# Optimization experiments

Hardware: AMD Instinct MI355X
Metric: run time of the kernel (lower is better)

The kernel has to match this reference:

```python
import math
import jax, jax.numpy as jnp
import numpy as np

B, S, D, H, DK = 2, 2048, 1024, 16, 64
NUM_BUCKETS, MAX_DISTANCE = 32, 128


def _relative_position_bucket(rel_pos):
    # bidirectional=True (encoder): is_decoder=False
    nb = NUM_BUCKETS // 2
    rel_buckets = (rel_pos > 0).astype(jnp.int32) * nb
    rp = jnp.abs(rel_pos)
    max_exact = nb // 2
    is_small = rp < max_exact
    rp_large = max_exact + (
        jnp.log(rp.astype(jnp.float32) / max_exact)
        / math.log(MAX_DISTANCE / max_exact)
        * (nb - max_exact)
    ).astype(jnp.int32)
    rp_large = jnp.minimum(rp_large, nb - 1)
    return rel_buckets + jnp.where(is_small, rp, rp_large)


def compute_bias(rel_bias, q_len, k_len):
    ctx = jnp.arange(q_len, dtype=jnp.int32)[:, None]
    mem = jnp.arange(k_len, dtype=jnp.int32)[None, :]
    buckets = _relative_position_bucket(mem - ctx)          # [q,k]
    vals = rel_bias[buckets]                                 # [q,k,H]
    return jnp.transpose(vals, (2, 0, 1))[None]              # [1,H,q,k]


def setup_inputs() -> dict:
    key = jax.random.key(0)
    ks = jax.random.split(key, 6)
    scale = 0.02
    return {
        "hidden_states": jax.random.normal(ks[0], (B, S, D), jnp.float32),
        "Wq": jax.random.normal(ks[1], (D, H * DK), jnp.float32) * scale,
        "Wk": jax.random.normal(ks[2], (D, H * DK), jnp.float32) * scale,
        "Wv": jax.random.normal(ks[3], (D, H * DK), jnp.float32) * scale,
        "Wo": jax.random.normal(ks[4], (H * DK, D), jnp.float32) * scale,
        "rel_bias": jax.random.normal(ks[5], (NUM_BUCKETS, H), jnp.float32) * scale,
    }


def reference(hidden_states, Wq, Wk, Wv, Wo, rel_bias):
    b, s, _ = hidden_states.shape

    def shape(x):  # [b,s,H*DK] -> [b,H,s,DK]
        return x.reshape(b, s, H, DK).transpose(0, 2, 1, 3)

    q = shape(hidden_states @ Wq)
    k = shape(hidden_states @ Wk)
    v = shape(hidden_states @ Wv)

    # T5: no 1/sqrt(d_k) scaling
    scores = jnp.einsum("bhqd,bhkd->bhqk", q, k)
    position_bias = compute_bias(rel_bias, s, s)             # [1,H,s,s]
    scores = scores + position_bias
    attn = jax.nn.softmax(scores.astype(jnp.float32), axis=-1).astype(scores.dtype)
    out = jnp.einsum("bhqk,bhkd->bhqd", attn, v)
    out = out.transpose(0, 2, 1, 3).reshape(b, s, H * DK)
    return out @ Wo
```

## Files before the change

### kernel.cpp

```cpp
#include <hip/hip_runtime.h>

#define HH 16
#define DKK 64
#define SS 2048
#define BB 2
#define DD 1024

typedef __attribute__((ext_vector_type(4))) float f32x4;
typedef __attribute__((ext_vector_type(16))) float f32x16;
typedef __attribute__((ext_vector_type(8))) short bf16x8;
typedef __attribute__((ext_vector_type(4))) short s16x4;
typedef __attribute__((ext_vector_type(4))) int i32x4;

#define WAITCNT_VM0 0xF70

__device__ __forceinline__ short bf16b(float f) {
    union { float f; unsigned u; } x; x.f = f;
    unsigned r = (x.u + 0x7fffu + ((x.u >> 16) & 1u)) >> 16;
    return (short)r;
}

__device__ __forceinline__ f32x4 mfma16(bf16x8 a, bf16x8 b, f32x4 c) {
    return __builtin_amdgcn_mfma_f32_16x16x32_bf16(a, b, c, 0, 0, 0);
}

__device__ __forceinline__ f32x16 mfma32(bf16x8 a, bf16x8 b, f32x16 c) {
    return __builtin_amdgcn_mfma_f32_32x32x16_bf16(a, b, c, 0, 0, 0);
}

__device__ __forceinline__ void lds16(const short* g, short* l) {
    __builtin_amdgcn_global_load_lds(
        (const __attribute__((address_space(1))) void*)g,
        (__attribute__((address_space(3))) void*)l, 16, 0, 0);
}

__device__ __forceinline__ int cvtpk(float lo, float hi) {
    int r;
    asm("v_cvt_pk_bf16_f32 %0, %1, %2" : "=v"(r) : "v"(lo), "v"(hi));
    return r;
}

__device__ __forceinline__ void swap32(int& a, int& b) {
    asm("v_permlane32_swap_b32 %0, %1" : "+v"(a), "+v"(b));
}

__global__ __launch_bounds__(256) void prep(
    const float* __restrict__ hs,
    const float* __restrict__ W0, const float* __restrict__ W1,
    const float* __restrict__ W2, const float* __restrict__ W3,
    const float* __restrict__ rb,
    short* __restrict__ hsb,
    short* __restrict__ T0, short* __restrict__ T1,
    short* __restrict__ T2, short* __restrict__ T3,
    float* __restrict__ tab) {
    __shared__ short tile[32][33];
    int blk = blockIdx.x, tid = threadIdx.x;
    if (blk < 4096) {
        int i = (blk * 256 + tid) * 4;
        f32x4 v = *(const f32x4*)(hs + i);
        s16x4 o;
        o.x = bf16b(v.x); o.y = bf16b(v.y); o.z = bf16b(v.z); o.w = bf16b(v.w);
        *(s16x4*)(hsb + i) = o;
    } else if (blk < 8192) {
        int t = blk - 4096;
        int z = t >> 10, r = t & 1023;
        int bx = r & 31, by = r >> 5;
        const float* W; short* T;
        switch (z) {
            case 0: W = W0; T = T0; break;
            case 1: W = W1; T = T1; break;
            case 2: W = W2; T = T2; break;
            default: W = W3; T = T3; break;
        }
        int n0 = bx * 32, k0 = by * 32;
        int tx = tid & 31, ty = (tid >> 5) * 4;
#pragma unroll
        for (int i = 0; i < 4; i++)
            tile[ty + i][tx] = bf16b(W[(k0 + ty + i) * DD + n0 + tx]);
        __syncthreads();
#pragma unroll
        for (int i = 0; i < 4; i++)
            T[(n0 + ty + i) * DD + k0 + tx] = tile[tx][ty + i];
    } else {
        int idx = (blk - 8192) * 256 + tid;
        if (idx < HH * 4095) {
            int h = idx / 4095, d = idx % 4095;
            int rel = d - 2047;
            int bucket = (rel > 0) ? 16 : 0;
            unsigned rr = (rel < 0) ? (unsigned)(-rel) : (unsigned)rel;
            int add;
            if (rr < 8) add = (int)rr;
            else {
                int e = 31 - __clz(rr);
                unsigned long long r2 = (unsigned long long)rr * (unsigned long long)rr;
                int f = 2 * e + ((r2 >= (2ull << (2 * e))) ? 1 : 0);
                add = 8 + (f - 6);
                if (add > 15) add = 15;
            }
            bucket += add;
            tab[h * 4095 + d] = rb[bucket * HH + h] * 1.44269504f;
        }
    }
}

__global__ __launch_bounds__(256) void gemm_qkv(
    const short* __restrict__ A, const short* __restrict__ Wt,
    short* __restrict__ Cq, short* __restrict__ Ck, short* __restrict__ Cvt) {
    const int K = 1024;
    __shared__ short As[128 * 32];
    __shared__ short Bs[128 * 32];
    int tid = threadIdx.x;
    int wave = tid >> 6, lane = tid & 63;
    int quad = lane >> 4, l16 = lane & 15;
    int m0 = blockIdx.y * 128, n0 = blockIdx.x * 128;

    int wm = (wave & 1) * 64, wn = (wave >> 1) * 64;
    int r0 = tid >> 2, c0 = (tid & 3) * 8;

    f32x4 acc[4][4];
#pragma unroll
    for (int i = 0; i < 4; i++)
#pragma unroll
        for (int j = 0; j < 4; j++) acc[i][j] = (f32x4){0.f, 0.f, 0.f, 0.f};

    for (int k0 = 0; k0 < K; k0 += 32) {
        __syncthreads();
        lds16(A + (size_t)(m0 + r0) * K + k0 + c0, As + wave * 512);
        lds16(A + (size_t)(m0 + 64 + r0) * K + k0 + c0, As + 2048 + wave * 512);
        lds16(Wt + (size_t)(n0 + r0) * K + k0 + c0, Bs + wave * 512);
        lds16(Wt + (size_t)(n0 + 64 + r0) * K + k0 + c0, Bs + 2048 + wave * 512);
        __syncthreads();
        bf16x8 af[4], bfr[4];
#pragma unroll
        for (int t = 0; t < 4; t++) {
            af[t] = *(const bf16x8*)(As + (wm + t * 16 + l16) * 32 + quad * 8);
            bfr[t] = *(const bf16x8*)(Bs + (wn + t * 16 + l16) * 32 + quad * 8);
        }
#pragma unroll
        for (int mt = 0; mt < 4; mt++)
#pragma unroll
            for (int nt = 0; nt < 4; nt++)
                acc[mt][nt] = mfma16(af[mt], bfr[nt], acc[mt][nt]);
    }

#pragma unroll
    for (int mt = 0; mt < 4; mt++) {
#pragma unroll
        for (int nt = 0; nt < 4; nt++) {
#pragma unroll
            for (int r = 0; r < 4; r++) {
                int gm = m0 + wm + mt * 16 + quad * 4 + r;
                int gn = n0 + wn + nt * 16 + l16;
                int b = gm >> 11, s = gm & 2047;
                int which = gn >> 10;
                int h = (gn >> 6) & 15, dk = gn & 63;
                short bv = bf16b(acc[mt][nt][r]);
                if (which == 0)
                    Cq[(((size_t)(b * HH + h)) * SS + s) * DKK + dk] = bv;
                else if (which == 1)
                    Ck[(((size_t)(b * HH + h)) * SS + s) * DKK + dk] = bv;
                else
                    Cvt[(((size_t)(b * HH + h)) * DKK + dk) * SS + s] = bv;
            }
        }
    }
}

__global__ __launch_bounds__(256) void gemm_out(
    const short* __restrict__ A, const short* __restrict__ Wt,
    float* __restrict__ Cout) {
    const int K = 1024, N = 1024;
    __shared__ short As[64 * 32];
    __shared__ short Bs[128 * 32];
    int tid = threadIdx.x;
    int wave = tid >> 6, lane = tid & 63;
    int quad = lane >> 4, l16 = lane & 15;
    int m0 = blockIdx.y * 64, n0 = blockIdx.x * 128;

    int wm = (wave & 1) * 32, wn = (wave >> 1) * 64;
    int r0 = tid >> 2, c0 = (tid & 3) * 8;

    f32x4 acc[2][4];
#pragma unroll
    for (int i = 0; i < 2; i++)
#pragma unroll
        for (int j = 0; j < 4; j++) acc[i][j] = (f32x4){0.f, 0.f, 0.f, 0.f};

    for (int k0 = 0; k0 < K; k0 += 32) {
        __syncthreads();
        lds16(A + (size_t)(m0 + r0) * K + k0 + c0, As + wave * 512);
        lds16(Wt + (size_t)(n0 + r0) * K + k0 + c0, Bs + wave * 512);
        lds16(Wt + (size_t)(n0 + 64 + r0) * K + k0 + c0, Bs + 2048 + wave * 512);
        __syncthreads();
        bf16x8 af[2], bfr[4];
#pragma unroll
        for (int t = 0; t < 2; t++)
            af[t] = *(const bf16x8*)(As + (wm + t * 16 + l16) * 32 + quad * 8);
#pragma unroll
        for (int t = 0; t < 4; t++)
            bfr[t] = *(const bf16x8*)(Bs + (wn + t * 16 + l16) * 32 + quad * 8);
#pragma unroll
        for (int mt = 0; mt < 2; mt++)
#pragma unroll
            for (int nt = 0; nt < 4; nt++)
                acc[mt][nt] = mfma16(af[mt], bfr[nt], acc[mt][nt]);
    }

#pragma unroll
    for (int mt = 0; mt < 2; mt++)
#pragma unroll
        for (int nt = 0; nt < 4; nt++)
#pragma unroll
            for (int r = 0; r < 4; r++) {
                int gm = m0 + wm + mt * 16 + quad * 4 + r;
                int gn = n0 + wn + nt * 16 + l16;
                Cout[(size_t)gm * N + gn] = acc[mt][nt][r];
            }
}

__global__ __launch_bounds__(256, 2) void attn(
    const short* __restrict__ Q, const short* __restrict__ Kmat,
    const short* __restrict__ Vt, const float* __restrict__ btab,
    short* __restrict__ O) {
    __shared__ short Ks[2][64 * 64];
    __shared__ short Vs[2][64 * 64];
    __shared__ float Linv[4][32];

    int tid = threadIdx.x;
    int wave = tid >> 6, lane = tid & 63;
    int el = lane & 31, hi = lane >> 5;
    int ex7 = el & 7;
    int bh = blockIdx.x;
    int h = bh & 15, b = bh >> 4;
    int q0b = blockIdx.y * 128;
    int q0w = q0b + wave * 32;

    const short* Qb = Q + (size_t)bh * SS * DKK;
    const short* Kb = Kmat + (size_t)bh * SS * DKK;
    const short* Vb = Vt + (size_t)bh * DKK * SS;
    const float* bt = btab + h * 4095;

    float blo = bt[2047 - 128];
    float bhi = bt[2047 + 128];

    int kro = tid >> 3;
    int gk = (tid & 7) ^ (kro & 7);
    const short* Kg0 = Kb + (size_t)kro * DKK + gk * 8;
    const short* Kg1 = Kb + (size_t)(kro + 32) * DKK + gk * 8;
    const short* Vg0 = Vb + (size_t)kro * SS + gk * 8;
    const short* Vg1 = Vb + (size_t)(kro + 32) * SS + gk * 8;

    bf16x8 qB[4];
#pragma unroll
    for (int c = 0; c < 4; c++)
        qB[c] = *(const bf16x8*)(Qb + (size_t)(q0w + el) * DKK + c * 16 + hi * 8);

    f32x16 o0, o1;
#pragma unroll
    for (int i = 0; i < 16; i++) { o0[i] = 0.f; o1[i] = 0.f; }
    float ls0 = 0.f, ls1 = 0.f, ls2 = 0.f, ls3 = 0.f;

    int bq = 2047 - q0w - el;

    lds16(Kg0, &Ks[0][wave * 512]);
    lds16(Kg1, &Ks[0][2048 + wave * 512]);
    lds16(Vg0, &Vs[0][wave * 512]);
    lds16(Vg1, &Vs[0][2048 + wave * 512]);

    int cur = 0;
    for (int kc = 0; kc < SS; kc += 64) {
        __syncthreads();
        int kn = (kc + 64) & (SS - 1);
        int nxt = cur ^ 1;
        lds16(Kg0 + (size_t)kn * DKK, &Ks[nxt][wave * 512]);
        lds16(Kg1 + (size_t)kn * DKK, &Ks[nxt][2048 + wave * 512]);
        lds16(Vg0 + kn, &Vs[nxt][wave * 512]);
        lds16(Vg1 + kn, &Vs[nxt][2048 + wave * 512]);

        const short* Ksc = &Ks[cur][0];
        const short* Vsc = &Vs[cur][0];

        bf16x8 vf[4][2];
#pragma unroll
        for (int c4 = 0; c4 < 4; c4++)
#pragma unroll
            for (int m = 0; m < 2; m++)
                vf[c4][m] = *(const bf16x8*)(
                    Vsc + (m * 32 + el) * 64 + (((2 * c4 + hi) ^ ex7) * 8));

#pragma unroll
        for (int st = 0; st < 2; st++) {
            f32x16 acc;
#pragma unroll
            for (int i = 0; i < 16; i++) acc[i] = 0.f;
#pragma unroll
            for (int c = 0; c < 4; c++) {
                bf16x8 kA = *(const bf16x8*)(
                    Ksc + (st * 32 + el) * 64 + (((2 * c + hi) ^ ex7) * 8));
                acc = mfma32(kA, qB[c], acc);
            }

            int ks = kc + st * 32;
            float br[16];
            if (ks > q0w - 159 && ks < q0w + 159) {
#pragma unroll
                for (int r = 0; r < 16; r++)
                    br[r] = bt[bq + ks + ((r & 3) + 8 * (r >> 2) + 4 * hi)];
            } else {
                float bc = (ks <= q0w - 159) ? blo : bhi;
#pragma unroll
                for (int r = 0; r < 16; r++) br[r] = bc;
            }

            float p[16];
#pragma unroll
            for (int r = 0; r < 16; r++)
                p[r] = __builtin_amdgcn_exp2f(
                    fmaf(acc[r], 1.44269504f, br[r]));
#pragma unroll
            for (int r = 0; r < 16; r += 4) {
                ls0 += p[r]; ls1 += p[r + 1]; ls2 += p[r + 2]; ls3 += p[r + 3];
            }

            int A1 = cvtpk(p[0], p[1]),   A2 = cvtpk(p[2], p[3]);
            int B1 = cvtpk(p[4], p[5]),   B2 = cvtpk(p[6], p[7]);
            int C1 = cvtpk(p[8], p[9]),   C2 = cvtpk(p[10], p[11]);
            int D1 = cvtpk(p[12], p[13]), D2 = cvtpk(p[14], p[15]);
            swap32(A1, B1); swap32(A2, B2);
            swap32(C1, D1); swap32(C2, D2);
            bf16x8 pf0 = __builtin_bit_cast(bf16x8, (i32x4){A1, A2, B1, B2});
            bf16x8 pf1 = __builtin_bit_cast(bf16x8, (i32x4){C1, C2, D1, D2});

            o0 = mfma32(pf0, vf[st * 2 + 0][0], o0);
            o1 = mfma32(pf0, vf[st * 2 + 0][1], o1);
            o0 = mfma32(pf1, vf[st * 2 + 1][0], o0);
            o1 = mfma32(pf1, vf[st * 2 + 1][1], o1);
        }
        cur ^= 1;
    }
    __builtin_amdgcn_s_waitcnt(WAITCNT_VM0);

    float lsum = (ls0 + ls1) + (ls2 + ls3);
    float tot = lsum + __shfl_xor(lsum, 32);
    float inv = 1.f / tot;
    if (hi == 0) Linv[wave][el] = inv;
    __asm__ __volatile__("" ::: "memory");

#pragma unroll
    for (int r = 0; r < 16; r++) {
        int qm = (r & 3) + 8 * (r >> 2) + 4 * hi;
        float iv = Linv[wave][qm];
        size_t base = ((size_t)(b * SS + q0w + qm)) * (HH * DKK) + h * DKK;
        O[base + el] = bf16b(o0[r] * iv);
        O[base + 32 + el] = bf16b(o1[r] * iv);
    }
}

extern "C" void kernel_launch(void* const* d_in, const int* in_sizes, int n_in,
                              void* d_out, int out_size, void* d_ws, size_t ws_size,
                              hipStream_t stream) {
    const float* hs = (const float*)d_in[0];
    const float* Wq = (const float*)d_in[1];
    const float* Wk = (const float*)d_in[2];
    const float* Wv = (const float*)d_in[3];
    const float* Wo = (const float*)d_in[4];
    const float* rb = (const float*)d_in[5];
    float* out = (float*)d_out;

    char* ws = (char*)d_ws;
    size_t off = 0;
    auto alloc = [&](size_t bytes) -> void* {
        void* p = (void*)(ws + off);
        off += (bytes + 255) & ~(size_t)255;
        return p;
    };
    const size_t M = (size_t)BB * SS;
    short* hsb = (short*)alloc(M * DD * 2);
    short* WqT = (short*)alloc((size_t)DD * DD * 2);
    short* WkT = (short*)alloc((size_t)DD * DD * 2);
    short* WvT = (short*)alloc((size_t)DD * DD * 2);
    short* WoT = (short*)alloc((size_t)DD * DD * 2);
    short* Qb  = (short*)alloc(M * DD * 2);
    short* Kb  = (short*)alloc(M * DD * 2);
    short* VTb = (short*)alloc(M * DD * 2);
    short* Ab  = (short*)alloc(M * DD * 2);
    float* btab = (float*)alloc((size_t)HH * 4095 * 4);

    prep<<<8448, 256, 0, stream>>>(hs, Wq, Wk, Wv, Wo, rb,
                                   hsb, WqT, WkT, WvT, WoT, btab);
    gemm_qkv<<<dim3(24, 32), 256, 0, stream>>>(hsb, WqT, Qb, Kb, VTb);
    attn<<<dim3(32, 16), 256, 0, stream>>>(Qb, Kb, VTb, btab, Ab);
    gemm_out<<<dim3(8, 64), 256, 0, stream>>>(Ab, WoT, out);
}
```

Before: 193.2 us.

## Load V fragments directly from global into registers, drop V LDS staging

```diff
diff --git a/kernel.cpp b/kernel.cpp
--- a/kernel.cpp
+++ b/kernel.cpp
@@ -223,7 +223,6 @@
     const short* __restrict__ Vt, const float* __restrict__ btab,
     short* __restrict__ O) {
     __shared__ short Ks[2][64 * 64];
-    __shared__ short Vs[2][64 * 64];
     __shared__ float Linv[4][32];
 
     int tid = threadIdx.x;
@@ -247,8 +246,9 @@
     int gk = (tid & 7) ^ (kro & 7);
     const short* Kg0 = Kb + (size_t)kro * DKK + gk * 8;
     const short* Kg1 = Kb + (size_t)(kro + 32) * DKK + gk * 8;
-    const short* Vg0 = Vb + (size_t)kro * SS + gk * 8;
-    const short* Vg1 = Vb + (size_t)(kro + 32) * SS + gk * 8;
+
+    const short* Vrow0 = Vb + (size_t)el * SS + hi * 8;
+    const short* Vrow1 = Vb + (size_t)(32 + el) * SS + hi * 8;
 
     bf16x8 qB[4];
 #pragma unroll
@@ -264,41 +264,42 @@
 
     lds16(Kg0, &Ks[0][wave * 512]);
     lds16(Kg1, &Ks[0][2048 + wave * 512]);
-    lds16(Vg0, &Vs[0][wave * 512]);
-    lds16(Vg1, &Vs[0][2048 + wave * 512]);
+
+    bf16x8 vfA[4][2], vfB[4][2];
+#pragma unroll
+    for (int c4 = 0; c4 < 4; c4++) {
+        vfA[c4][0] = *(const bf16x8*)(Vrow0 + c4 * 16);
+        vfA[c4][1] = *(const bf16x8*)(Vrow1 + c4 * 16);
+    }
 
     int cur = 0;
-    for (int kc = 0; kc < SS; kc += 64) {
+    auto iter = [&](int kc, bf16x8 (&vfc)[4][2], bf16x8 (&vfn)[4][2]) {
         __syncthreads();
         int kn = (kc + 64) & (SS - 1);
         int nxt = cur ^ 1;
         lds16(Kg0 + (size_t)kn * DKK, &Ks[nxt][wave * 512]);
         lds16(Kg1 + (size_t)kn * DKK, &Ks[nxt][2048 + wave * 512]);
-        lds16(Vg0 + kn, &Vs[nxt][wave * 512]);
-        lds16(Vg1 + kn, &Vs[nxt][2048 + wave * 512]);
+#pragma unroll
+        for (int c4 = 0; c4 < 4; c4++) {
+            vfn[c4][0] = *(const bf16x8*)(Vrow0 + kn + c4 * 16);
+            vfn[c4][1] = *(const bf16x8*)(Vrow1 + kn + c4 * 16);
+        }
 
         const short* Ksc = &Ks[cur][0];
-        const short* Vsc = &Vs[cur][0];
-
-        bf16x8 vf[4][2];
-#pragma unroll
-        for (int c4 = 0; c4 < 4; c4++)
-#pragma unroll
-            for (int m = 0; m < 2; m++)
-                vf[c4][m] = *(const bf16x8*)(
-                    Vsc + (m * 32 + el) * 64 + (((2 * c4 + hi) ^ ex7) * 8));
 
 #pragma unroll
         for (int st = 0; st < 2; st++) {
             f32x16 acc;
 #pragma unroll
             for (int i = 0; i < 16; i++) acc[i] = 0.f;
+            __builtin_amdgcn_s_setprio(1);
 #pragma unroll
             for (int c = 0; c < 4; c++) {
                 bf16x8 kA = *(const bf16x8*)(
                     Ksc + (st * 32 + el) * 64 + (((2 * c + hi) ^ ex7) * 8));
                 acc = mfma32(kA, qB[c], acc);
             }
+            __builtin_amdgcn_s_setprio(0);
 
             int ks = kc + st * 32;
             float br[16];
@@ -331,12 +332,19 @@
             bf16x8 pf0 = __builtin_bit_cast(bf16x8, (i32x4){A1, A2, B1, B2});
             bf16x8 pf1 = __builtin_bit_cast(bf16x8, (i32x4){C1, C2, D1, D2});
 
-            o0 = mfma32(pf0, vf[st * 2 + 0][0], o0);
-            o1 = mfma32(pf0, vf[st * 2 + 0][1], o1);
-            o0 = mfma32(pf1, vf[st * 2 + 1][0], o0);
-            o1 = mfma32(pf1, vf[st * 2 + 1][1], o1);
+            __builtin_amdgcn_s_setprio(1);
+            o0 = mfma32(pf0, vfc[st * 2 + 0][0], o0);
+            o1 = mfma32(pf0, vfc[st * 2 + 0][1], o1);
+            o0 = mfma32(pf1, vfc[st * 2 + 1][0], o0);
+            o1 = mfma32(pf1, vfc[st * 2 + 1][1], o1);
+            __builtin_amdgcn_s_setprio(0);
         }
         cur ^= 1;
+    };
+
+    for (int kc = 0; kc < SS; kc += 128) {
+        iter(kc, vfA, vfB);
+        iter(kc + 64, vfB, vfA);
     }
     __builtin_amdgcn_s_waitcnt(WAITCNT_VM0);
 
```

Result: slower. 231.6 us (+19.9%).

## Process two 32-row query tiles per wave in attention to reuse K/V fragments

Applied to the files above, without the earlier changes.

```diff
diff --git a/kernel.cpp b/kernel.cpp
--- a/kernel.cpp
+++ b/kernel.cpp
@@ -218,13 +218,13 @@
             }
 }
 
-__global__ __launch_bounds__(256, 2) void attn(
+__global__ __launch_bounds__(256, 1) void attn(
     const short* __restrict__ Q, const short* __restrict__ Kmat,
     const short* __restrict__ Vt, const float* __restrict__ btab,
     short* __restrict__ O) {
     __shared__ short Ks[2][64 * 64];
     __shared__ short Vs[2][64 * 64];
-    __shared__ float Linv[4][32];
+    __shared__ float Linv[4][64];
 
     int tid = threadIdx.x;
     int wave = tid >> 6, lane = tid & 63;
@@ -232,8 +232,8 @@
     int ex7 = el & 7;
     int bh = blockIdx.x;
     int h = bh & 15, b = bh >> 4;
-    int q0b = blockIdx.y * 128;
-    int q0w = q0b + wave * 32;
+    int q0b = blockIdx.y * 256;
+    int q0w = q0b + wave * 64;
 
     const short* Qb = Q + (size_t)bh * SS * DKK;
     const short* Kb = Kmat + (size_t)bh * SS * DKK;
@@ -250,17 +250,28 @@
     const short* Vg0 = Vb + (size_t)kro * SS + gk * 8;
     const short* Vg1 = Vb + (size_t)(kro + 32) * SS + gk * 8;
 
-    bf16x8 qB[4];
-#pragma unroll
-    for (int c = 0; c < 4; c++)
-        qB[c] = *(const bf16x8*)(Qb + (size_t)(q0w + el) * DKK + c * 16 + hi * 8);
-
-    f32x16 o0, o1;
-#pragma unroll
-    for (int i = 0; i < 16; i++) { o0[i] = 0.f; o1[i] = 0.f; }
-    float ls0 = 0.f, ls1 = 0.f, ls2 = 0.f, ls3 = 0.f;
-
-    int bq = 2047 - q0w - el;
+    bf16x8 qB[2][4];
+#pragma unroll
+    for (int qt = 0; qt < 2; qt++)
+#pragma unroll
+        for (int c = 0; c < 4; c++)
+            qB[qt][c] = *(const bf16x8*)(
+                Qb + (size_t)(q0w + qt * 32 + el) * DKK + c * 16 + hi * 8);
+
+    f32x16 o[2][2];
+#pragma unroll
+    for (int qt = 0; qt < 2; qt++)
+#pragma unroll
+        for (int m = 0; m < 2; m++)
+#pragma unroll
+            for (int i = 0; i < 16; i++) o[qt][m][i] = 0.f;
+    float ls[2][4];
+#pragma unroll
+    for (int qt = 0; qt < 2; qt++)
+#pragma unroll
+        for (int i = 0; i < 4; i++) ls[qt][i] = 0.f;
+
+    int bq[2] = {2047 - q0w - el, 2047 - (q0w + 32) - el};
 
     lds16(Kg0, &Ks[0][wave * 512]);
     lds16(Kg1, &Ks[0][2048 + wave * 512]);
@@ -290,70 +301,88 @@
 
 #pragma unroll
         for (int st = 0; st < 2; st++) {
-            f32x16 acc;
-#pragma unroll
-            for (int i = 0; i < 16; i++) acc[i] = 0.f;
-#pragma unroll
-            for (int c = 0; c < 4; c++) {
-                bf16x8 kA = *(const bf16x8*)(
+            bf16x8 kA[4];
+#pragma unroll
+            for (int c = 0; c < 4; c++)
+                kA[c] = *(const bf16x8*)(
                     Ksc + (st * 32 + el) * 64 + (((2 * c + hi) ^ ex7) * 8));
-                acc = mfma32(kA, qB[c], acc);
+            int ks = kc + st * 32;
+
+#pragma unroll
+            for (int qt = 0; qt < 2; qt++) {
+                int q0 = q0w + qt * 32;
+                f32x16 acc;
+#pragma unroll
+                for (int i = 0; i < 16; i++) acc[i] = 0.f;
+                __builtin_amdgcn_s_setprio(1);
+#pragma unroll
+                for (int c = 0; c < 4; c++)
+                    acc = mfma32(kA[c], qB[qt][c], acc);
+                __builtin_amdgcn_s_setprio(0);
+
+                float br[16];
+                if (ks > q0 - 159 && ks < q0 + 159) {
+#pragma unroll
+                    for (int r = 0; r < 16; r++)
+                        br[r] = bt[bq[qt] + ks + ((r & 3) + 8 * (r >> 2) + 4 * hi)];
+                } else {
+                    float bc = (ks <= q0 - 159) ? blo : bhi;
+#pragma unroll
+                    for (int r = 0; r < 16; r++) br[r] = bc;
+                }
+
+                float p[16];
+#pragma unroll
+                for (int r = 0; r < 16; r++)
+                    p[r] = __builtin_amdgcn_exp2f(
+                        fmaf(acc[r], 1.44269504f, br[r]));
+#pragma unroll
+                for (int r = 0; r < 16; r += 4) {
+                    ls[qt][0] += p[r];     ls[qt][1] += p[r + 1];
+                    ls[qt][2] += p[r + 2]; ls[qt][3] += p[r + 3];
+                }
+
+                int A1 = cvtpk(p[0], p[1]),   A2 = cvtpk(p[2], p[3]);
+                int B1 = cvtpk(p[4], p[5]),   B2 = cvtpk(p[6], p[7]);
+                int C1 = cvtpk(p[8], p[9]),   C2 = cvtpk(p[10], p[11]);
+                int D1 = cvtpk(p[12], p[13]), D2 = cvtpk(p[14], p[15]);
+                swap32(A1, B1); swap32(A2, B2);
+                swap32(C1, D1); swap32(C2, D2);
+                bf16x8 pf0 = __builtin_bit_cast(bf16x8, (i32x4){A1, A2, B1, B2});
+                bf16x8 pf1 = __builtin_bit_cast(bf16x8, (i32x4){C1, C2, D1, D2});
+
+                __builtin_amdgcn_s_setprio(1);
+                o[qt][0] = mfma32(pf0, vf[st * 2 + 0][0], o[qt][0]);
+                o[qt][1] = mfma32(pf0, vf[st * 2 + 0][1], o[qt][1]);
+                o[qt][0] = mfma32(pf1, vf[st * 2 + 1][0], o[qt][0]);
+                o[qt][1] = mfma32(pf1, vf[st * 2 + 1][1], o[qt][1]);
+                __builtin_amdgcn_s_setprio(0);
             }
-
-            int ks = kc + st * 32;
-            float br[16];
-            if (ks > q0w - 159 && ks < q0w + 159) {
-#pragma unroll
-                for (int r = 0; r < 16; r++)
-                    br[r] = bt[bq + ks + ((r & 3) + 8 * (r >> 2) + 4 * hi)];
-            } else {
-                float bc = (ks <= q0w - 159) ? blo : bhi;
-#pragma unroll
-                for (int r = 0; r < 16; r++) br[r] = bc;
-            }
-
-            float p[16];
-#pragma unroll
-            for (int r = 0; r < 16; r++)
-                p[r] = __builtin_amdgcn_exp2f(
-                    fmaf(acc[r], 1.44269504f, br[r]));
-#pragma unroll
-            for (int r = 0; r < 16; r += 4) {
-                ls0 += p[r]; ls1 += p[r + 1]; ls2 += p[r + 2]; ls3 += p[r + 3];
-            }
-
-            int A1 = cvtpk(p[0], p[1]),   A2 = cvtpk(p[2], p[3]);
-            int B1 = cvtpk(p[4], p[5]),   B2 = cvtpk(p[6], p[7]);
-            int C1 = cvtpk(p[8], p[9]),   C2 = cvtpk(p[10], p[11]);
-            int D1 = cvtpk(p[12], p[13]), D2 = cvtpk(p[14], p[15]);
-            swap32(A1, B1); swap32(A2, B2);
-            swap32(C1, D1); swap32(C2, D2);
-            bf16x8 pf0 = __builtin_bit_cast(bf16x8, (i32x4){A1, A2, B1, B2});
-            bf16x8 pf1 = __builtin_bit_cast(bf16x8, (i32x4){C1, C2, D1, D2});
-
-            o0 = mfma32(pf0, vf[st * 2 + 0][0], o0);
-            o1 = mfma32(pf0, vf[st * 2 + 0][1], o1);
-            o0 = mfma32(pf1, vf[st * 2 + 1][0], o0);
-            o1 = mfma32(pf1, vf[st * 2 + 1][1], o1);
         }
         cur ^= 1;
     }
     __builtin_amdgcn_s_waitcnt(WAITCNT_VM0);
 
-    float lsum = (ls0 + ls1) + (ls2 + ls3);
-    float tot = lsum + __shfl_xor(lsum, 32);
-    float inv = 1.f / tot;
-    if (hi == 0) Linv[wave][el] = inv;
+#pragma unroll
+    for (int qt = 0; qt < 2; qt++) {
+        float lsum = (ls[qt][0] + ls[qt][1]) + (ls[qt][2] + ls[qt][3]);
+        float tot = lsum + __shfl_xor(lsum, 32);
+        float inv = 1.f / tot;
+        if (hi == 0) Linv[wave][qt * 32 + el] = inv;
+    }
     __asm__ __volatile__("" ::: "memory");
 
 #pragma unroll
-    for (int r = 0; r < 16; r++) {
-        int qm = (r & 3) + 8 * (r >> 2) + 4 * hi;
-        float iv = Linv[wave][qm];
-        size_t base = ((size_t)(b * SS + q0w + qm)) * (HH * DKK) + h * DKK;
-        O[base + el] = bf16b(o0[r] * iv);
-        O[base + 32 + el] = bf16b(o1[r] * iv);
-    }
+    for (int qt = 0; qt < 2; qt++)
+#pragma unroll
+        for (int r = 0; r < 16; r++) {
+            int qm = (r & 3) + 8 * (r >> 2) + 4 * hi;
+            float iv = Linv[wave][qt * 32 + qm];
+            size_t base =
+                ((size_t)(b * SS + q0w + qt * 32 + qm)) * (HH * DKK) + h * DKK;
+            O[base + el] = bf16b(o[qt][0][r] * iv);
+            O[base + 32 + el] = bf16b(o[qt][1][r] * iv);
+        }
 }
 
 extern "C" void kernel_launch(void* const* d_in, const int* in_sizes, int n_in,
@@ -389,6 +418,6 @@
     prep<<<8448, 256, 0, stream>>>(hs, Wq, Wk, Wv, Wo, rb,
                                    hsb, WqT, WkT, WvT, WoT, btab);
     gemm_qkv<<<dim3(24, 32), 256, 0, stream>>>(hsb, WqT, Qb, Kb, VTb);
-    attn<<<dim3(32, 16), 256, 0, stream>>>(Qb, Kb, VTb, btab, Ab);
+    attn<<<dim3(32, 8), 256, 0, stream>>>(Qb, Kb, VTb, btab, Ab);
     gemm_out<<<dim3(8, 64), 256, 0, stream>>>(Ab, WoT, out);
 }
```

Result: slower. 212.6 us (+10.1%).

## Split attention key range across two wave groups and merge partial outputs in LDS

Applied to the files above, without the earlier changes.

```diff
diff --git a/kernel.cpp b/kernel.cpp
--- a/kernel.cpp
+++ b/kernel.cpp
@@ -218,22 +218,23 @@
             }
 }
 
-__global__ __launch_bounds__(256, 2) void attn(
+__global__ __launch_bounds__(512, 4) void attn(
     const short* __restrict__ Q, const short* __restrict__ Kmat,
     const short* __restrict__ Vt, const float* __restrict__ btab,
     short* __restrict__ O) {
-    __shared__ short Ks[2][64 * 64];
-    __shared__ short Vs[2][64 * 64];
-    __shared__ float Linv[4][32];
+    __shared__ short Ks[2][2][64 * 64];
+    __shared__ short Vs[2][2][64 * 64];
 
     int tid = threadIdx.x;
     int wave = tid >> 6, lane = tid & 63;
+    int w4 = wave & 3, half = wave >> 2;
     int el = lane & 31, hi = lane >> 5;
     int ex7 = el & 7;
     int bh = blockIdx.x;
     int h = bh & 15, b = bh >> 4;
     int q0b = blockIdx.y * 128;
-    int q0w = q0b + wave * 32;
+    int q0w = q0b + w4 * 32;
+    int ko = half * 1024;
 
     const short* Qb = Q + (size_t)bh * SS * DKK;
     const short* Kb = Kmat + (size_t)bh * SS * DKK;
@@ -243,12 +244,13 @@
     float blo = bt[2047 - 128];
     float bhi = bt[2047 + 128];
 
-    int kro = tid >> 3;
-    int gk = (tid & 7) ^ (kro & 7);
-    const short* Kg0 = Kb + (size_t)kro * DKK + gk * 8;
-    const short* Kg1 = Kb + (size_t)(kro + 32) * DKK + gk * 8;
-    const short* Vg0 = Vb + (size_t)kro * SS + gk * 8;
-    const short* Vg1 = Vb + (size_t)(kro + 32) * SS + gk * 8;
+    int tid2 = tid & 255;
+    int kro = tid2 >> 3;
+    int gk = (tid2 & 7) ^ (kro & 7);
+    const short* Kg0 = Kb + (size_t)(ko + kro) * DKK + gk * 8;
+    const short* Kg1 = Kb + (size_t)(ko + kro + 32) * DKK + gk * 8;
+    const short* Vg0 = Vb + (size_t)kro * SS + ko + gk * 8;
+    const short* Vg1 = Vb + (size_t)(kro + 32) * SS + ko + gk * 8;
 
     bf16x8 qB[4];
 #pragma unroll
@@ -262,23 +264,23 @@
 
     int bq = 2047 - q0w - el;
 
-    lds16(Kg0, &Ks[0][wave * 512]);
-    lds16(Kg1, &Ks[0][2048 + wave * 512]);
-    lds16(Vg0, &Vs[0][wave * 512]);
-    lds16(Vg1, &Vs[0][2048 + wave * 512]);
+    lds16(Kg0, &Ks[half][0][w4 * 512]);
+    lds16(Kg1, &Ks[half][0][2048 + w4 * 512]);
+    lds16(Vg0, &Vs[half][0][w4 * 512]);
+    lds16(Vg1, &Vs[half][0][2048 + w4 * 512]);
 
     int cur = 0;
-    for (int kc = 0; kc < SS; kc += 64) {
-        __syncthreads();
-        int kn = (kc + 64) & (SS - 1);
+    for (int kc2 = 0; kc2 < 1024; kc2 += 64) {
+        __syncthreads();
+        int kn2 = (kc2 + 64) & 1023;
         int nxt = cur ^ 1;
-        lds16(Kg0 + (size_t)kn * DKK, &Ks[nxt][wave * 512]);
-        lds16(Kg1 + (size_t)kn * DKK, &Ks[nxt][2048 + wave * 512]);
-        lds16(Vg0 + kn, &Vs[nxt][wave * 512]);
-        lds16(Vg1 + kn, &Vs[nxt][2048 + wave * 512]);
-
-        const short* Ksc = &Ks[cur][0];
-        const short* Vsc = &Vs[cur][0];
+        lds16(Kg0 + (size_t)kn2 * DKK, &Ks[half][nxt][w4 * 512]);
+        lds16(Kg1 + (size_t)kn2 * DKK, &Ks[half][nxt][2048 + w4 * 512]);
+        lds16(Vg0 + kn2, &Vs[half][nxt][w4 * 512]);
+        lds16(Vg1 + kn2, &Vs[half][nxt][2048 + w4 * 512]);
+
+        const short* Ksc = &Ks[half][cur][0];
+        const short* Vsc = &Vs[half][cur][0];
 
         bf16x8 vf[4][2];
 #pragma unroll
@@ -293,14 +295,16 @@
             f32x16 acc;
 #pragma unroll
             for (int i = 0; i < 16; i++) acc[i] = 0.f;
+            __builtin_amdgcn_s_setprio(1);
 #pragma unroll
             for (int c = 0; c < 4; c++) {
                 bf16x8 kA = *(const bf16x8*)(
                     Ksc + (st * 32 + el) * 64 + (((2 * c + hi) ^ ex7) * 8));
                 acc = mfma32(kA, qB[c], acc);
             }
-
-            int ks = kc + st * 32;
+            __builtin_amdgcn_s_setprio(0);
+
+            int ks = ko + kc2 + st * 32;
             float br[16];
             if (ks > q0w - 159 && ks < q0w + 159) {
 #pragma unroll
@@ -331,28 +335,51 @@
             bf16x8 pf0 = __builtin_bit_cast(bf16x8, (i32x4){A1, A2, B1, B2});
             bf16x8 pf1 = __builtin_bit_cast(bf16x8, (i32x4){C1, C2, D1, D2});
 
+            __builtin_amdgcn_s_setprio(1);
             o0 = mfma32(pf0, vf[st * 2 + 0][0], o0);
             o1 = mfma32(pf0, vf[st * 2 + 0][1], o1);
             o0 = mfma32(pf1, vf[st * 2 + 1][0], o0);
             o1 = mfma32(pf1, vf[st * 2 + 1][1], o1);
+            __builtin_amdgcn_s_setprio(0);
         }
         cur ^= 1;
     }
     __builtin_amdgcn_s_waitcnt(WAITCNT_VM0);
 
     float lsum = (ls0 + ls1) + (ls2 + ls3);
-    float tot = lsum + __shfl_xor(lsum, 32);
-    float inv = 1.f / tot;
-    if (hi == 0) Linv[wave][el] = inv;
-    __asm__ __volatile__("" ::: "memory");
-
-#pragma unroll
-    for (int r = 0; r < 16; r++) {
-        int qm = (r & 3) + 8 * (r >> 2) + 4 * hi;
-        float iv = Linv[wave][qm];
-        size_t base = ((size_t)(b * SS + q0w + qm)) * (HH * DKK) + h * DKK;
-        O[base + el] = bf16b(o0[r] * iv);
-        O[base + 32 + el] = bf16b(o1[r] * iv);
+    float toth = lsum + __shfl_xor(lsum, 32);
+
+    __syncthreads();
+
+    float* Ob = (float*)&Ks[0][0][0];
+    float* Ls = (float*)&Vs[0][0][0];
+    int ex5 = lane & 31;
+    int obase = (w4 * 64 + lane) * 32;
+
+    if (half == 1) {
+        if (hi == 0) Ls[w4 * 32 + el] = toth;
+#pragma unroll
+        for (int j = 0; j < 16; j++) {
+            Ob[obase + (j ^ ex5)] = o0[j];
+            Ob[obase + ((16 + j) ^ ex5)] = o1[j];
+        }
+    }
+    __syncthreads();
+    if (half == 0) {
+        float tot = toth + Ls[w4 * 32 + el];
+        if (hi == 0) Ls[128 + w4 * 32 + el] = 1.f / tot;
+        __asm__ __volatile__("" ::: "memory");
+#pragma unroll
+        for (int r = 0; r < 16; r++) {
+            int qm = (r & 3) + 8 * (r >> 2) + 4 * hi;
+            float iv = Ls[128 + w4 * 32 + qm];
+            float a0 = o0[r] + Ob[obase + (r ^ ex5)];
+            float a1 = o1[r] + Ob[obase + ((16 + r) ^ ex5)];
+            size_t base =
+                ((size_t)(b * SS + q0w + qm)) * (HH * DKK) + h * DKK;
+            O[base + el] = bf16b(a0 * iv);
+            O[base + 32 + el] = bf16b(a1 * iv);
+        }
     }
 }
 
@@ -389,6 +416,6 @@
     prep<<<8448, 256, 0, stream>>>(hs, Wq, Wk, Wv, Wo, rb,
                                    hsb, WqT, WkT, WvT, WoT, btab);
     gemm_qkv<<<dim3(24, 32), 256, 0, stream>>>(hsb, WqT, Qb, Kb, VTb);
-    attn<<<dim3(32, 16), 256, 0, stream>>>(Qb, Kb, VTb, btab, Ab);
+    attn<<<dim3(32, 16), 512, 0, stream>>>(Qb, Kb, VTb, btab, Ab);
     gemm_out<<<dim3(8, 64), 256, 0, stream>>>(Ab, WoT, out);
 }
```

Result: slower. 213.5 us (+10.5%).
